# Kernel optimization log

Measured on AMD Instinct MI355X. Metric: run time of the kernel, lower is better.

Reference implementation:

```python
import jax, jax.numpy as jnp
import numpy as np

B, V, D, K = 32, 4096, 64, 512


def setup_inputs() -> dict:
    key = jax.random.key(0)
    k1, k2 = jax.random.split(key)
    z_e = jax.random.normal(k1, (B, V, D), dtype=jnp.float32)
    # nn.Embedding weight initialized uniform(-1/K, 1/K)
    emb = jax.random.uniform(k2, (K, D), dtype=jnp.float32, minval=-1.0 / K, maxval=1.0 / K)
    return {"z_e": z_e, "emb": emb}


def reference(z_e, emb):
    b, v, d = z_e.shape
    flat = z_e.reshape(-1, d)  # [N, D], N = B*V
    # Squared Euclidean distances via dot-product expansion.
    # torch.cdist returns sqrt of this, but argmin is identical (monotone sqrt).
    d2 = (
        jnp.sum(flat * flat, axis=-1, keepdims=True)  # [N, 1]
        - 2.0 * flat @ emb.T                          # [N, K]
        + jnp.sum(emb * emb, axis=-1)                 # [K]
    )
    indices = jnp.argmin(d2, axis=1)                  # [N]
    z_q = emb[indices].reshape(z_e.shape)             # [B, V, D]
    z_q_st = z_e + jax.lax.stop_gradient(z_q - z_e)   # straight-through
    return z_q_st, z_q, indices.reshape(b, v)
```

## Files before the change

### kernel.cpp

```cpp
#include <hip/hip_runtime.h>


#define VQ_N (32 * 4096)
#define VQ_D 64
#define VQ_K 512

__device__ __forceinline__ float freeze(float x) {
  asm volatile("" : "+v"(x));
  return x;
}

__global__ __launch_bounds__(256) void vq_norms_kernel(
    const float* __restrict__ emb, float* __restrict__ nrm) {
  int k = blockIdx.x * blockDim.x + threadIdx.x;
  if (k < VQ_K) {
    const float* e = emb + k * VQ_D;
    float r0 = freeze(e[0] * e[0]), r1 = freeze(e[1] * e[1]);
    float r2 = freeze(e[2] * e[2]), r3 = freeze(e[3] * e[3]);
    float r4 = freeze(e[4] * e[4]), r5 = freeze(e[5] * e[5]);
    float r6 = freeze(e[6] * e[6]), r7 = freeze(e[7] * e[7]);
#pragma unroll
    for (int i = 8; i < VQ_D; i += 8) {
      r0 += freeze(e[i + 0] * e[i + 0]); r1 += freeze(e[i + 1] * e[i + 1]);
      r2 += freeze(e[i + 2] * e[i + 2]); r3 += freeze(e[i + 3] * e[i + 3]);
      r4 += freeze(e[i + 4] * e[i + 4]); r5 += freeze(e[i + 5] * e[i + 5]);
      r6 += freeze(e[i + 6] * e[i + 6]); r7 += freeze(e[i + 7] * e[i + 7]);
    }
    nrm[k] = ((r0 + r1) + (r2 + r3)) + ((r4 + r5) + (r6 + r7));
  }
}

__global__ __launch_bounds__(256) void vq_main_kernel(
    const float* __restrict__ z_e, const float* __restrict__ emb,
    const float* __restrict__ nrm, float* __restrict__ out_st,
    float* __restrict__ out_q, float* __restrict__ out_idx) {
  __shared__ float4 z_lds[16][64];
  __shared__ float4 e_lds[64 * 16];
  __shared__ float s_val[256];
  __shared__ int s_idx[256];
  __shared__ int s_best[64];

  const int tid = threadIdx.x;
  const int lane = tid & 63;
  const int wave = __builtin_amdgcn_readfirstlane(tid >> 6);
  const int row0 = blockIdx.x * 64;
  const int row = row0 + lane;

  const float4* zg = (const float4*)(z_e + (size_t)row0 * VQ_D);
#pragma unroll
  for (int t = 0; t < 4; ++t) {
    int i = t * 256 + tid;
    z_lds[i & 15][i >> 4] = zg[i];
  }
  __syncthreads();

  float r0, r1, r2, r3, r4, r5, r6, r7;
  {
    float4 p0 = z_lds[0][lane], p1 = z_lds[1][lane];
    r0 = freeze(p0.x * p0.x); r1 = freeze(p0.y * p0.y);
    r2 = freeze(p0.z * p0.z); r3 = freeze(p0.w * p0.w);
    r4 = freeze(p1.x * p1.x); r5 = freeze(p1.y * p1.y);
    r6 = freeze(p1.z * p1.z); r7 = freeze(p1.w * p1.w);
#pragma unroll
    for (int c = 2; c < 16; c += 2) {
      float4 q0 = z_lds[c][lane], q1 = z_lds[c + 1][lane];
      r0 += freeze(q0.x * q0.x); r1 += freeze(q0.y * q0.y);
      r2 += freeze(q0.z * q0.z); r3 += freeze(q0.w * q0.w);
      r4 += freeze(q1.x * q1.x); r5 += freeze(q1.y * q1.y);
      r6 += freeze(q1.z * q1.z); r7 += freeze(q1.w * q1.w);
    }
  }
  const float A = ((r0 + r1) + (r2 + r3)) + ((r4 + r5) + (r6 + r7));

  float bestv = 3.4e38f;
  int best = 0;

  for (int t = 0; t < 8; ++t) {
    const float4* eg = (const float4*)emb + (size_t)t * 1024;
#pragma unroll
    for (int i = 0; i < 4; ++i) e_lds[i * 256 + tid] = eg[i * 256 + tid];
    __syncthreads();

#pragma unroll
    for (int g = 0; g < 2; ++g) {
      const int kl = wave * 16 + g * 8;
      const int kk = t * 64 + kl;
      const float4* ep = &e_lds[kl * 16];
      float a0 = 0.f, a1 = 0.f, a2 = 0.f, a3 = 0.f;
      float a4 = 0.f, a5 = 0.f, a6 = 0.f, a7 = 0.f;
#define VQ_DOT4(ACC, J)                                                  \
  do {                                                                   \
    float4 f = ep[(J)*16 + c];                                           \
    ACC = fmaf(zc.x, f.x, ACC); ACC = fmaf(zc.y, f.y, ACC);              \
    ACC = fmaf(zc.z, f.z, ACC); ACC = fmaf(zc.w, f.w, ACC);              \
  } while (0)
#pragma unroll
      for (int c = 0; c < 16; ++c) {
        float4 zc = z_lds[c][lane];
        VQ_DOT4(a0, 0); VQ_DOT4(a1, 1); VQ_DOT4(a2, 2); VQ_DOT4(a3, 3);
        VQ_DOT4(a4, 4); VQ_DOT4(a5, 5); VQ_DOT4(a6, 6); VQ_DOT4(a7, 7);
      }
#undef VQ_DOT4
      float t0 = fmaf(-2.0f, a0, A) + nrm[kk + 0];
      float t1 = fmaf(-2.0f, a1, A) + nrm[kk + 1];
      float t2 = fmaf(-2.0f, a2, A) + nrm[kk + 2];
      float t3 = fmaf(-2.0f, a3, A) + nrm[kk + 3];
      float t4 = fmaf(-2.0f, a4, A) + nrm[kk + 4];
      float t5 = fmaf(-2.0f, a5, A) + nrm[kk + 5];
      float t6 = fmaf(-2.0f, a6, A) + nrm[kk + 6];
      float t7 = fmaf(-2.0f, a7, A) + nrm[kk + 7];
      if (t0 < bestv) { bestv = t0; best = kk + 0; }
      if (t1 < bestv) { bestv = t1; best = kk + 1; }
      if (t2 < bestv) { bestv = t2; best = kk + 2; }
      if (t3 < bestv) { bestv = t3; best = kk + 3; }
      if (t4 < bestv) { bestv = t4; best = kk + 4; }
      if (t5 < bestv) { bestv = t5; best = kk + 5; }
      if (t6 < bestv) { bestv = t6; best = kk + 6; }
      if (t7 < bestv) { bestv = t7; best = kk + 7; }
    }
    __syncthreads();
  }

  s_val[wave * 64 + lane] = bestv;
  s_idx[wave * 64 + lane] = best;
  __syncthreads();

  if (tid < 64) {
    float v = s_val[tid];
    int b = s_idx[tid];
#pragma unroll
    for (int c = 1; c < 4; ++c) {
      float vc = s_val[c * 64 + tid];
      int bc = s_idx[c * 64 + tid];
      if (vc < v || (vc == v && bc < b)) { v = vc; b = bc; }
    }
    s_best[tid] = b;
    out_idx[row] = (float)b;
  }
  __syncthreads();

  const float4* eg4 = (const float4*)emb;
  const size_t base4 = (size_t)blockIdx.x * 64 * 16;
  float4* o0 = (float4*)out_st;
  float4* o1 = (float4*)out_q;
#pragma unroll
  for (int t = 0; t < 4; ++t) {
    int i = t * 256 + tid;
    int r = i >> 4, j = i & 15;
    float4 v = eg4[s_best[r] * 16 + j];
    o0[base4 + i] = v;
    o1[base4 + i] = v;
  }
}

extern "C" void kernel_launch(void* const* d_in, const int* in_sizes, int n_in,
                              void* d_out, int out_size, void* d_ws,
                              size_t ws_size, hipStream_t stream) {
  const float* z_e = (const float*)d_in[0];
  const float* emb = (const float*)d_in[1];
  float* nrm = (float*)d_ws;

  float* out_st = (float*)d_out;
  float* out_q = out_st + (size_t)VQ_N * VQ_D;
  float* out_idx = out_q + (size_t)VQ_N * VQ_D;

  vq_norms_kernel<<<(VQ_K + 255) / 256, 256, 0, stream>>>(emb, nrm);
  vq_main_kernel<<<VQ_N / 64, 256, 0, stream>>>(z_e, emb, nrm, out_st, out_q,
                                                out_idx);
}
```

Before: 262.2 us.

## Register-tile distance GEMM with 4 rows x 16 codes per thread

Each block now handles 256 rows with 512 threads. Every thread keeps a 4x16 accumulator tile (4 rows, 16 codebook entries), so each LDS load of z and emb is reused across several FMAs instead of once per row. Codebook norms are staged in LDS, and per-row best candidates are reduced across 8 waves. The gains are higher arithmetic intensity per LDS read and fewer blocks in exchange for heavy register pressure (64 accumulators plus operands) with launch bounds requesting 2 blocks, which risks spilling or low occupancy.

```diff
diff --git a/kernel.cpp b/kernel.cpp
--- a/kernel.cpp
+++ b/kernel.cpp
@@ -4,6 +4,12 @@
 #define VQ_N (32 * 4096)
 #define VQ_D 64
 #define VQ_K 512
+#define ROWS 256
+#define THREADS 512
+#define TILE_K 128
+#define NT 4
+#define NR 16
+#define MR 4
 
 __device__ __forceinline__ float freeze(float x) {
   asm volatile("" : "+v"(x));
@@ -30,122 +36,131 @@
   }
 }
 
-__global__ __launch_bounds__(256) void vq_main_kernel(
+__global__ __launch_bounds__(THREADS, 2) void vq_main_kernel(
     const float* __restrict__ z_e, const float* __restrict__ emb,
     const float* __restrict__ nrm, float* __restrict__ out_st,
     float* __restrict__ out_q, float* __restrict__ out_idx) {
-  __shared__ float4 z_lds[16][64];
-  __shared__ float4 e_lds[64 * 16];
-  __shared__ float s_val[256];
-  __shared__ int s_idx[256];
-  __shared__ int s_best[64];
+  __shared__ float4 z_lds[16][ROWS];
+  __shared__ float4 e_lds[TILE_K * 16];
+  __shared__ float A_lds[ROWS];
+  __shared__ float nrm_lds[VQ_K];
 
   const int tid = threadIdx.x;
   const int lane = tid & 63;
-  const int wave = __builtin_amdgcn_readfirstlane(tid >> 6);
-  const int row0 = blockIdx.x * 64;
-  const int row = row0 + lane;
+  const int w = __builtin_amdgcn_readfirstlane(tid >> 6);
+  const size_t row0 = (size_t)blockIdx.x * ROWS;
 
-  const float4* zg = (const float4*)(z_e + (size_t)row0 * VQ_D);
+  const float4* zg = (const float4*)(z_e + row0 * VQ_D);
 #pragma unroll
-  for (int t = 0; t < 4; ++t) {
-    int i = t * 256 + tid;
+  for (int t = 0; t < 8; ++t) {
+    int i = t * THREADS + tid;
     z_lds[i & 15][i >> 4] = zg[i];
   }
+  nrm_lds[tid] = nrm[tid];
   __syncthreads();
 
-  float r0, r1, r2, r3, r4, r5, r6, r7;
-  {
-    float4 p0 = z_lds[0][lane], p1 = z_lds[1][lane];
-    r0 = freeze(p0.x * p0.x); r1 = freeze(p0.y * p0.y);
-    r2 = freeze(p0.z * p0.z); r3 = freeze(p0.w * p0.w);
-    r4 = freeze(p1.x * p1.x); r5 = freeze(p1.y * p1.y);
-    r6 = freeze(p1.z * p1.z); r7 = freeze(p1.w * p1.w);
+  if (tid < ROWS) {
+    float4 p0 = z_lds[0][tid], p1 = z_lds[1][tid];
+    float r0 = freeze(p0.x * p0.x), r1 = freeze(p0.y * p0.y);
+    float r2 = freeze(p0.z * p0.z), r3 = freeze(p0.w * p0.w);
+    float r4 = freeze(p1.x * p1.x), r5 = freeze(p1.y * p1.y);
+    float r6 = freeze(p1.z * p1.z), r7 = freeze(p1.w * p1.w);
 #pragma unroll
     for (int c = 2; c < 16; c += 2) {
-      float4 q0 = z_lds[c][lane], q1 = z_lds[c + 1][lane];
+      float4 q0 = z_lds[c][tid], q1 = z_lds[c + 1][tid];
       r0 += freeze(q0.x * q0.x); r1 += freeze(q0.y * q0.y);
       r2 += freeze(q0.z * q0.z); r3 += freeze(q0.w * q0.w);
       r4 += freeze(q1.x * q1.x); r5 += freeze(q1.y * q1.y);
       r6 += freeze(q1.z * q1.z); r7 += freeze(q1.w * q1.w);
     }
+    A_lds[tid] = ((r0 + r1) + (r2 + r3)) + ((r4 + r5) + (r6 + r7));
   }
-  const float A = ((r0 + r1) + (r2 + r3)) + ((r4 + r5) + (r6 + r7));
+  __syncthreads();
 
-  float bestv = 3.4e38f;
-  int best = 0;
+  float Ar[MR];
+#pragma unroll
+  for (int m = 0; m < MR; ++m) Ar[m] = A_lds[lane + 64 * m];
 
-  for (int t = 0; t < 8; ++t) {
-    const float4* eg = (const float4*)emb + (size_t)t * 1024;
+  float bestv[MR];
+  int besti[MR];
 #pragma unroll
-    for (int i = 0; i < 4; ++i) e_lds[i * 256 + tid] = eg[i * 256 + tid];
+  for (int m = 0; m < MR; ++m) { bestv[m] = 3.4e38f; besti[m] = 0; }
+
+  for (int t = 0; t < NT; ++t) {
+    const float4* eg = (const float4*)emb + (size_t)t * (TILE_K * 16);
+#pragma unroll
+    for (int i = 0; i < 4; ++i)
+      e_lds[i * THREADS + tid] = eg[i * THREADS + tid];
     __syncthreads();
 
+    float acc[MR][NR];
 #pragma unroll
-    for (int g = 0; g < 2; ++g) {
-      const int kl = wave * 16 + g * 8;
-      const int kk = t * 64 + kl;
-      const float4* ep = &e_lds[kl * 16];
-      float a0 = 0.f, a1 = 0.f, a2 = 0.f, a3 = 0.f;
-      float a4 = 0.f, a5 = 0.f, a6 = 0.f, a7 = 0.f;
-#define VQ_DOT4(ACC, J)                                                  \
-  do {                                                                   \
-    float4 f = ep[(J)*16 + c];                                           \
-    ACC = fmaf(zc.x, f.x, ACC); ACC = fmaf(zc.y, f.y, ACC);              \
-    ACC = fmaf(zc.z, f.z, ACC); ACC = fmaf(zc.w, f.w, ACC);              \
-  } while (0)
+    for (int m = 0; m < MR; ++m)
 #pragma unroll
-      for (int c = 0; c < 16; ++c) {
-        float4 zc = z_lds[c][lane];
-        VQ_DOT4(a0, 0); VQ_DOT4(a1, 1); VQ_DOT4(a2, 2); VQ_DOT4(a3, 3);
-        VQ_DOT4(a4, 4); VQ_DOT4(a5, 5); VQ_DOT4(a6, 6); VQ_DOT4(a7, 7);
+      for (int j = 0; j < NR; ++j) acc[m][j] = 0.f;
+
+#pragma unroll
+    for (int c = 0; c < 16; ++c) {
+      float4 zr[MR];
+#pragma unroll
+      for (int m = 0; m < MR; ++m) zr[m] = z_lds[c][lane + 64 * m];
+#pragma unroll
+      for (int j = 0; j < NR; ++j) {
+        float4 f = e_lds[(8 * j + w) * 16 + c];
+#pragma unroll
+        for (int m = 0; m < MR; ++m) {
+          acc[m][j] = fmaf(zr[m].x, f.x, acc[m][j]);
+          acc[m][j] = fmaf(zr[m].y, f.y, acc[m][j]);
+          acc[m][j] = fmaf(zr[m].z, f.z, acc[m][j]);
+          acc[m][j] = fmaf(zr[m].w, f.w, acc[m][j]);
+        }
       }
-#undef VQ_DOT4
-      float t0 = fmaf(-2.0f, a0, A) + nrm[kk + 0];
-      float t1 = fmaf(-2.0f, a1, A) + nrm[kk + 1];
-      float t2 = fmaf(-2.0f, a2, A) + nrm[kk + 2];
-      float t3 = fmaf(-2.0f, a3, A) + nrm[kk + 3];
-      float t4 = fmaf(-2.0f, a4, A) + nrm[kk + 4];
-      float t5 = fmaf(-2.0f, a5, A) + nrm[kk + 5];
-      float t6 = fmaf(-2.0f, a6, A) + nrm[kk + 6];
-      float t7 = fmaf(-2.0f, a7, A) + nrm[kk + 7];
-      if (t0 < bestv) { bestv = t0; best = kk + 0; }
-      if (t1 < bestv) { bestv = t1; best = kk + 1; }
-      if (t2 < bestv) { bestv = t2; best = kk + 2; }
-      if (t3 < bestv) { bestv = t3; best = kk + 3; }
-      if (t4 < bestv) { bestv = t4; best = kk + 4; }
-      if (t5 < bestv) { bestv = t5; best = kk + 5; }
-      if (t6 < bestv) { bestv = t6; best = kk + 6; }
-      if (t7 < bestv) { bestv = t7; best = kk + 7; }
+    }
+
+#pragma unroll
+    for (int j = 0; j < NR; ++j) {
+      const int k = t * TILE_K + 8 * j + w;
+      const float C = nrm_lds[k];
+#pragma unroll
+      for (int m = 0; m < MR; ++m) {
+        float tv = fmaf(-2.0f, acc[m][j], Ar[m]) + C;
+        if (tv < bestv[m]) { bestv[m] = tv; besti[m] = k; }
+      }
     }
     __syncthreads();
   }
 
-  s_val[wave * 64 + lane] = bestv;
-  s_idx[wave * 64 + lane] = best;
-  __syncthreads();
-
-  if (tid < 64) {
-    float v = s_val[tid];
-    int b = s_idx[tid];
+  float* sv = (float*)e_lds;
+  int* si = (int*)((float*)e_lds + 8 * ROWS);
 #pragma unroll
-    for (int c = 1; c < 4; ++c) {
-      float vc = s_val[c * 64 + tid];
-      int bc = s_idx[c * 64 + tid];
-      if (vc < v || (vc == v && bc < b)) { v = vc; b = bc; }
-    }
-    s_best[tid] = b;
-    out_idx[row] = (float)b;
+  for (int m = 0; m < MR; ++m) {
+    sv[w * ROWS + lane + 64 * m] = bestv[m];
+    si[w * ROWS + lane + 64 * m] = besti[m];
   }
   __syncthreads();
 
+  if (tid < ROWS) {
+    float v = sv[tid];
+    int b = si[tid];
+#pragma unroll
+    for (int q = 1; q < 8; ++q) {
+      float vq = sv[q * ROWS + tid];
+      int bq = si[q * ROWS + tid];
+      if (vq < v || (vq == v && bq < b)) { v = vq; b = bq; }
+    }
+    ((int*)A_lds)[tid] = b;
+    out_idx[row0 + tid] = (float)b;
+  }
+  __syncthreads();
+
+  const int* s_best = (const int*)A_lds;
   const float4* eg4 = (const float4*)emb;
-  const size_t base4 = (size_t)blockIdx.x * 64 * 16;
+  const size_t base4 = row0 * 16;
   float4* o0 = (float4*)out_st;
   float4* o1 = (float4*)out_q;
 #pragma unroll
-  for (int t = 0; t < 4; ++t) {
-    int i = t * 256 + tid;
+  for (int t = 0; t < 8; ++t) {
+    int i = t * THREADS + tid;
     int r = i >> 4, j = i & 15;
     float4 v = eg4[s_best[r] * 16 + j];
     o0[base4 + i] = v;
@@ -165,6 +180,6 @@
   float* out_idx = out_q + (size_t)VQ_N * VQ_D;
 
   vq_norms_kernel<<<(VQ_K + 255) / 256, 256, 0, stream>>>(emb, nrm);
-  vq_main_kernel<<<VQ_N / 64, 256, 0, stream>>>(z_e, emb, nrm, out_st, out_q,
-                                                out_idx);
+  vq_main_kernel<<<VQ_N / ROWS, THREADS, 0, stream>>>(z_e, emb, nrm, out_st,
+                                                      out_q, out_idx);
 }
```

After: 239.2 us. 1.1x faster.
